# Kernel tuning notes

Measured on AMD Instinct MI355X. Metric: run time of the kernel, lower is better.

## Reference

```python
import jax, jax.numpy as jnp
import numpy as np

B, S, T, D = 4, 512, 512, 256


def setup_inputs() -> dict:
    key = jax.random.key(0)
    ks = jax.random.split(key, 10)
    scale = 1.0 / np.sqrt(D)
    return {
        "source": jax.random.normal(ks[0], (B, S, D), jnp.float32),
        "target": jax.random.normal(ks[1], (B, T, D), jnp.float32),
        "W_src": jax.random.uniform(ks[2], (D, D), jnp.float32, -scale, scale),
        "b_src": jax.random.uniform(ks[3], (D,), jnp.float32, -scale, scale),
        "W_tgt": jax.random.uniform(ks[4], (D, D), jnp.float32, -scale, scale),
        "b_tgt": jax.random.uniform(ks[5], (D,), jnp.float32, -scale, scale),
        "W_res": jax.random.uniform(ks[6], (D, 1), jnp.float32, -scale, scale),
        "b_res": jax.random.uniform(ks[7], (1,), jnp.float32, -scale, scale),
        "W_prob": jax.random.uniform(ks[8], (D, 2), jnp.float32, -scale, scale),
        "b_prob": jax.random.uniform(ks[9], (2,), jnp.float32, -scale, scale),
    }


def reference(source, target, W_src, b_src, W_tgt, b_tgt, W_res, b_res, W_prob, b_prob):
    # source: (B,S,D), target: (B,T,D)
    src_lin = jnp.einsum("bsd,de->bse", source, W_src) + b_src  # (B,S,D)
    tgt_lin = jnp.einsum("btd,de->bte", target, W_tgt) + b_tgt  # (B,T,D)
    # Bahdanau-style additive attention: (B,T,S,D) broadcast, tanh, D->1
    h = jnp.tanh(src_lin[:, None, :, :] + tgt_lin[:, :, None, :])  # (B,T,S,D)
    genP = jnp.einsum("btsd,d->bts", h, W_res[:, 0]) + b_res[0]     # (B,T,S)
    prob = jax.nn.softmax(jnp.einsum("btd,de->bte", target, W_prob) + b_prob, axis=-1)  # (B,T,2)
    return genP, prob
```

## Files before the change

kernel.cpp:

```cpp
#include <hip/hip_runtime.h>

#define B_ 4
#define S_ 512
#define T_ 512
#define D_ 256
#define NSRC (B_ * S_)
#define K2F 2.8853900817779268f

typedef __attribute__((ext_vector_type(8))) short short8;
typedef __attribute__((ext_vector_type(4))) float f32x4;
typedef __attribute__((ext_vector_type(2))) float f32x2;

__device__ __forceinline__ unsigned short f2bf(float f) {
    union { float f; unsigned u; } v; v.f = f;
    unsigned r = v.u + 0x7FFF + ((v.u >> 16) & 1);
    return (unsigned short)(r >> 16);
}

__global__ __launch_bounds__(256) void prep_kernel(
    const float* __restrict__ src, const float* __restrict__ tgt,
    const float* __restrict__ Wsrc, const float* __restrict__ Wtgt,
    const float* __restrict__ Wp, const float* __restrict__ bp,
    unsigned short* __restrict__ abf, unsigned short* __restrict__ wtb,
    float* __restrict__ out)
{
    __shared__ float tl[64 * 65];
    const int blk = blockIdx.x, tid = threadIdx.x;

    if (blk < 1024) {
        int i4 = blk * 256 + tid;
        const int half = NSRC * D_ / 4;
        const float4* in = (i4 < half) ? (const float4*)src : (const float4*)tgt;
        int j = (i4 < half) ? i4 : i4 - half;
        float4 v = in[j];
        ushort4 o;
        o.x = f2bf(v.x); o.y = f2bf(v.y); o.z = f2bf(v.z); o.w = f2bf(v.w);
        *(ushort4*)&abf[i4 * 4] = o;
    } else if (blk < 1056) {
        int wb = blk - 1024;
        int e = wb >> 4, ti = wb & 15, tr = ti >> 2, tc = ti & 3;
        int r0 = tr * 64, c0 = tc * 64;
        const float* W = e ? Wtgt : Wsrc;
        #pragma unroll
        for (int it = 0; it < 4; it++) {
            int rr = (tid >> 4) + it * 16;
            int cc = (tid & 15) * 4;
            float4 v = *(const float4*)&W[(r0 + rr) * D_ + c0 + cc];
            tl[(cc + 0) * 65 + rr] = v.x;
            tl[(cc + 1) * 65 + rr] = v.y;
            tl[(cc + 2) * 65 + rr] = v.z;
            tl[(cc + 3) * 65 + rr] = v.w;
        }
        __syncthreads();
        #pragma unroll
        for (int it = 0; it < 2; it++) {
            int jj = (tid >> 3) + it * 32;
            int kk = (tid & 7) * 8;
            ushort4 lo, hi;
            lo.x = f2bf(tl[jj * 65 + kk + 0]); lo.y = f2bf(tl[jj * 65 + kk + 1]);
            lo.z = f2bf(tl[jj * 65 + kk + 2]); lo.w = f2bf(tl[jj * 65 + kk + 3]);
            hi.x = f2bf(tl[jj * 65 + kk + 4]); hi.y = f2bf(tl[jj * 65 + kk + 5]);
            hi.z = f2bf(tl[jj * 65 + kk + 6]); hi.w = f2bf(tl[jj * 65 + kk + 7]);
            int idx = (e * 256 + c0 + jj) * D_ + r0 + kk;
            *(ushort4*)&wtb[idx] = lo;
            *(ushort4*)&wtb[idx + 4] = hi;
        }
    } else {
        int row  = (blk - 1056) * 4 + (tid >> 6);
        int lane = tid & 63;
        float p0 = 0.f, p1 = 0.f;
        #pragma unroll
        for (int i = 0; i < 4; i++) {
            int d = lane + i * 64;
            float v = tgt[row * D_ + d];
            float2 w = *(const float2*)&Wp[d * 2];
            p0 = fmaf(v, w.x, p0);
            p1 = fmaf(v, w.y, p1);
        }
        #pragma unroll
        for (int off = 32; off > 0; off >>= 1) {
            p0 += __shfl_down(p0, off, 64);
            p1 += __shfl_down(p1, off, 64);
        }
        if (lane == 0) {
            const float L2E = 1.4426950408889634f;
            float l0 = p0 + bp[0], l1 = p1 + bp[1];
            float e10 = __builtin_amdgcn_exp2f((l1 - l0) * L2E);
            float e01 = __builtin_amdgcn_exp2f((l0 - l1) * L2E);
            out[B_ * T_ * S_ + row * 2 + 0] = __builtin_amdgcn_rcpf(1.f + e10);
            out[B_ * T_ * S_ + row * 2 + 1] = __builtin_amdgcn_rcpf(1.f + e01);
        }
    }
}

__global__ __launch_bounds__(256) void linT_kernel(
    const unsigned short* __restrict__ abf, const unsigned short* __restrict__ wtb,
    const float* __restrict__ bsrc, const float* __restrict__ btgt,
    float* __restrict__ yaT, float* __restrict__ ycT)
{
    int wid  = blockIdx.x * 4 + (threadIdx.x >> 6);
    int lane = threadIdx.x & 63;
    int rg = wid >> 3;
    int cg = wid & 7;
    int e  = rg >> 7;
    int r0 = rg * 16;
    int n = lane & 15, quad = lane >> 4;

    const float* bias = e ? btgt : bsrc;
    float* outT = e ? ycT : yaT;
    int orow0 = r0 - e * NSRC;

    int ct0 = cg * 2, ct1 = cg * 2 + 1;
    f32x4 acc0 = {0.f, 0.f, 0.f, 0.f};
    f32x4 acc1 = {0.f, 0.f, 0.f, 0.f};

    const unsigned short* aP  = &abf[(r0 + n) * D_ + quad * 8];
    const unsigned short* b0P = &wtb[(e * 256 + ct0 * 16 + n) * D_ + quad * 8];
    const unsigned short* b1P = &wtb[(e * 256 + ct1 * 16 + n) * D_ + quad * 8];

    #pragma unroll
    for (int ks = 0; ks < 8; ks++) {
        short8 a  = *(const short8*)&aP[ks * 32];
        short8 b0 = *(const short8*)&b0P[ks * 32];
        short8 b1 = *(const short8*)&b1P[ks * 32];
        acc0 = __builtin_amdgcn_mfma_f32_16x16x32_bf16(a, b0, acc0, 0, 0, 0);
        acc1 = __builtin_amdgcn_mfma_f32_16x16x32_bf16(a, b1, acc1, 0, 0, 0);
    }

    float b0v = bias[ct0 * 16 + n];
    float b1v = bias[ct1 * 16 + n];
    float4 o0, o1;
    o0.x = __builtin_amdgcn_exp2f((acc0[0] + b0v) * K2F);
    o0.y = __builtin_amdgcn_exp2f((acc0[1] + b0v) * K2F);
    o0.z = __builtin_amdgcn_exp2f((acc0[2] + b0v) * K2F);
    o0.w = __builtin_amdgcn_exp2f((acc0[3] + b0v) * K2F);
    o1.x = __builtin_amdgcn_exp2f((acc1[0] + b1v) * K2F);
    o1.y = __builtin_amdgcn_exp2f((acc1[1] + b1v) * K2F);
    o1.z = __builtin_amdgcn_exp2f((acc1[2] + b1v) * K2F);
    o1.w = __builtin_amdgcn_exp2f((acc1[3] + b1v) * K2F);
    *(float4*)&outT[(ct0 * 16 + n) * NSRC + orow0 + quad * 4] = o0;
    *(float4*)&outT[(ct1 * 16 + n) * NSRC + orow0 + quad * 4] = o1;
}

#define GSTR 68
__global__ __launch_bounds__(1024, 4) void genp_kernel(
    const float* __restrict__ yaT, const float* __restrict__ ycT,
    const float* __restrict__ Wres, const float* __restrict__ bres,
    float* __restrict__ out)
{
    __shared__ float lbuf[2 * 64 * GSTR];
    float* ls = lbuf;
    float* lt = lbuf + 64 * GSTR;
    __shared__ float c0s;

    const int tid = threadIdx.x;
    const int lane = tid & 63, w = tid >> 6;
    const int s0 = blockIdx.x * 64;
    const int t0 = blockIdx.y * 64;
    const int b  = blockIdx.z;
    const int sg = b * S_ + s0;
    const int tg = b * T_ + t0;

    if (w == 0) {
        float s = Wres[lane] + Wres[lane + 64] + Wres[lane + 128] + Wres[lane + 192];
        #pragma unroll
        for (int off = 32; off > 0; off >>= 1) s += __shfl_xor(s, off, 64);
        if (lane == 0) c0s = s + bres[0];
    }

    const int q = w >> 2;
    const int m = lane & 15;
    const int g = (w & 3) * 4 + (lane >> 4);
    const int dbase = q * 16;

    f32x2 acc[4][2];
    #pragma unroll
    for (int i = 0; i < 4; i++) {
        acc[i][0] = (f32x2){0.f, 0.f};
        acc[i][1] = (f32x2){0.f, 0.f};
    }

    for (int c = 0; c < 4; c++) {
        __syncthreads();
        #pragma unroll
        for (int j = 0; j < 8; j++) {
            int r = w * 8 + j;
            if (r < 64) ls[r * GSTR + lane] = yaT[(c * 64 + r) * NSRC + sg + lane];
            else        lt[(r - 64) * GSTR + lane] = ycT[(c * 64 + r - 64) * NSRC + tg + lane];
        }
        __syncthreads();

        const float* wp = &Wres[c * 64 + dbase];
        const f32x2 one2 = {1.f, 1.f};
        #pragma unroll
        for (int kp = 0; kp < 8; kp++) {
            const int d0 = dbase + 2 * kp, d1 = d0 + 1;
            float4 av0 = *(const float4*)&ls[d0 * GSTR + 4 * m];
            float4 av1 = *(const float4*)&ls[d1 * GSTR + 4 * m];
            float4 cv0 = *(const float4*)&lt[d0 * GSTR + 4 * g];
            float4 cv1 = *(const float4*)&lt[d1 * GSTR + 4 * g];
            const float w0 = wp[2 * kp], w1 = wp[2 * kp + 1];
            const f32x2 w0v = {w0, w0}, w1v = {w1, w1};
            f32x2 a0p[2] = {{av0.x, av0.y}, {av0.z, av0.w}};
            f32x2 a1p[2] = {{av1.x, av1.y}, {av1.z, av1.w}};
            const float cc0[4] = {cv0.x, cv0.y, cv0.z, cv0.w};
            const float cc1[4] = {cv1.x, cv1.y, cv1.z, cv1.w};
            #pragma unroll
            for (int i = 0; i < 4; i++) {
                const f32x2 c0v = {cc0[i], cc0[i]};
                const f32x2 c1v = {cc1[i], cc1[i]};
                #pragma unroll
                for (int jp = 0; jp < 2; jp++) {
                    f32x2 dd0 = a0p[jp] * c0v + one2;
                    f32x2 dd1 = a1p[jp] * c1v + one2;
                    f32x2 den = dd0 * dd1;
                    f32x2 tnu = dd0 * w1v;
                    f32x2 num = dd1 * w0v + tnu;
                    f32x2 r;
                    r.x = __builtin_amdgcn_rcpf(den.x);
                    r.y = __builtin_amdgcn_rcpf(den.y);
                    acc[i][jp] = num * r + acc[i][jp];
                }
            }
        }
    }

    __syncthreads();
    const int slot = ((w & 3) * 64 + lane) * 17;
    const int slotH = ((q >> 1) * 256 + (w & 3) * 64 + lane) * 17;
    if (q == 1 || q == 3) {
        #pragma unroll
        for (int i = 0; i < 4; i++) {
            float4 p = {acc[i][0].x, acc[i][0].y, acc[i][1].x, acc[i][1].y};
            *(float4*)&lbuf[slotH + 4 * i] = p;
        }
    }
    __syncthreads();
    if (q == 0 || q == 2) {
        #pragma unroll
        for (int i = 0; i < 4; i++) {
            float4 p = *(const float4*)&lbuf[slotH + 4 * i];
            acc[i][0].x += p.x; acc[i][0].y += p.y;
            acc[i][1].x += p.z; acc[i][1].y += p.w;
        }
    }
    __syncthreads();
    if (q == 2) {
        #pragma unroll
        for (int i = 0; i < 4; i++) {
            float4 p = {acc[i][0].x, acc[i][0].y, acc[i][1].x, acc[i][1].y};
            *(float4*)&lbuf[slot + 4 * i] = p;
        }
    }
    __syncthreads();
    if (q == 0) {
        const float C0 = c0s;
        #pragma unroll
        for (int i = 0; i < 4; i++) {
            float4 p = *(const float4*)&lbuf[slot + 4 * i];
            float4 o;
            o.x = C0 - 2.f * (acc[i][0].x + p.x);
            o.y = C0 - 2.f * (acc[i][0].y + p.y);
            o.z = C0 - 2.f * (acc[i][1].x + p.z);
            o.w = C0 - 2.f * (acc[i][1].y + p.w);
            *(float4*)&out[(b * T_ + t0 + 4 * g + i) * S_ + s0 + 4 * m] = o;
        }
    }
}

extern "C" void kernel_launch(void* const* d_in, const int* in_sizes, int n_in,
                              void* d_out, int out_size, void* d_ws, size_t ws_size,
                              hipStream_t stream) {
    const float* source = (const float*)d_in[0];
    const float* target = (const float*)d_in[1];
    const float* W_src  = (const float*)d_in[2];
    const float* b_src  = (const float*)d_in[3];
    const float* W_tgt  = (const float*)d_in[4];
    const float* b_tgt  = (const float*)d_in[5];
    const float* W_res  = (const float*)d_in[6];
    const float* b_res  = (const float*)d_in[7];
    const float* W_prob = (const float*)d_in[8];
    const float* b_prob = (const float*)d_in[9];
    float* out = (float*)d_out;

    unsigned short* abf = (unsigned short*)d_ws;
    unsigned short* wtb = abf + 2 * NSRC * D_;
    float* yaT = (float*)(wtb + 2 * D_ * D_);
    float* ycT = yaT + D_ * NSRC;

    prep_kernel<<<1568, 256, 0, stream>>>(source, target, W_src, W_tgt,
                                          W_prob, b_prob, abf, wtb, out);
    linT_kernel<<<512, 256, 0, stream>>>(abf, wtb, b_src, b_tgt, yaT, ycT);
    genp_kernel<<<dim3(8, 8, 4), 1024, 0, stream>>>(yaT, ycT, W_res, b_res, out);
}
```

Measured before the change: 118.8 us.

## Restructure linear MFMA tiles to keep weight fragments in registers across row tiles

The linear-projection kernel now swaps MFMA operands so the weight tile sits in the A slot. Each wave loads a 16-column weight slice once into registers and reuses it across four 16-row activation tiles, instead of loading one activation tile and two weight tiles per wave. The transposed outputs are now written as coalesced scalar stores along the row dimension, and the grid is halved. This reduces redundant weight loads and improves store coalescing, at the cost of fewer waves in flight for latency hiding.

```diff
diff --git a/kernel.cpp b/kernel.cpp
--- a/kernel.cpp
+++ b/kernel.cpp
@@ -98,48 +98,41 @@
     const float* __restrict__ bsrc, const float* __restrict__ btgt,
     float* __restrict__ yaT, float* __restrict__ ycT)
 {
-    int wid  = blockIdx.x * 4 + (threadIdx.x >> 6);
-    int lane = threadIdx.x & 63;
-    int rg = wid >> 3;
-    int cg = wid & 7;
-    int e  = rg >> 7;
-    int r0 = rg * 16;
-    int n = lane & 15, quad = lane >> 4;
+    const int W    = blockIdx.x * 4 + (threadIdx.x >> 6);
+    const int lane = threadIdx.x & 63;
+    const int rgrp = W >> 4;
+    const int dg   = W & 15;
+    const int e    = rgrp >> 5;
+    const int R0   = rgrp * 64;
+    const int orow0 = R0 - e * NSRC;
+    const int d0   = dg * 16;
+    const int n = lane & 15, quad = lane >> 4;
 
     const float* bias = e ? btgt : bsrc;
     float* outT = e ? ycT : yaT;
-    int orow0 = r0 - e * NSRC;
-
-    int ct0 = cg * 2, ct1 = cg * 2 + 1;
-    f32x4 acc0 = {0.f, 0.f, 0.f, 0.f};
-    f32x4 acc1 = {0.f, 0.f, 0.f, 0.f};
-
-    const unsigned short* aP  = &abf[(r0 + n) * D_ + quad * 8];
-    const unsigned short* b0P = &wtb[(e * 256 + ct0 * 16 + n) * D_ + quad * 8];
-    const unsigned short* b1P = &wtb[(e * 256 + ct1 * 16 + n) * D_ + quad * 8];
-
+
+    const unsigned short* aP = &wtb[(e * 256 + d0 + n) * D_ + quad * 8];
+    short8 af[8];
     #pragma unroll
-    for (int ks = 0; ks < 8; ks++) {
-        short8 a  = *(const short8*)&aP[ks * 32];
-        short8 b0 = *(const short8*)&b0P[ks * 32];
-        short8 b1 = *(const short8*)&b1P[ks * 32];
-        acc0 = __builtin_amdgcn_mfma_f32_16x16x32_bf16(a, b0, acc0, 0, 0, 0);
-        acc1 = __builtin_amdgcn_mfma_f32_16x16x32_bf16(a, b1, acc1, 0, 0, 0);
-    }
-
-    float b0v = bias[ct0 * 16 + n];
-    float b1v = bias[ct1 * 16 + n];
-    float4 o0, o1;
-    o0.x = __builtin_amdgcn_exp2f((acc0[0] + b0v) * K2F);
-    o0.y = __builtin_amdgcn_exp2f((acc0[1] + b0v) * K2F);
-    o0.z = __builtin_amdgcn_exp2f((acc0[2] + b0v) * K2F);
-    o0.w = __builtin_amdgcn_exp2f((acc0[3] + b0v) * K2F);
-    o1.x = __builtin_amdgcn_exp2f((acc1[0] + b1v) * K2F);
-    o1.y = __builtin_amdgcn_exp2f((acc1[1] + b1v) * K2F);
-    o1.z = __builtin_amdgcn_exp2f((acc1[2] + b1v) * K2F);
-    o1.w = __builtin_amdgcn_exp2f((acc1[3] + b1v) * K2F);
-    *(float4*)&outT[(ct0 * 16 + n) * NSRC + orow0 + quad * 4] = o0;
-    *(float4*)&outT[(ct1 * 16 + n) * NSRC + orow0 + quad * 4] = o1;
+    for (int ks = 0; ks < 8; ks++) af[ks] = *(const short8*)&aP[ks * 32];
+
+    const float4 vb = *(const float4*)&bias[d0 + quad * 4];
+
+    #pragma unroll
+    for (int f = 0; f < 4; f++) {
+        const unsigned short* bP = &abf[(R0 + 16 * f + n) * D_ + quad * 8];
+        f32x4 acc = {0.f, 0.f, 0.f, 0.f};
+        #pragma unroll
+        for (int ks = 0; ks < 8; ks++) {
+            short8 bf = *(const short8*)&bP[ks * 32];
+            acc = __builtin_amdgcn_mfma_f32_16x16x32_bf16(af[ks], bf, acc, 0, 0, 0);
+        }
+        const int rbase = orow0 + 16 * f + n;
+        outT[(d0 + quad * 4 + 0) * NSRC + rbase] = __builtin_amdgcn_exp2f((acc[0] + vb.x) * K2F);
+        outT[(d0 + quad * 4 + 1) * NSRC + rbase] = __builtin_amdgcn_exp2f((acc[1] + vb.y) * K2F);
+        outT[(d0 + quad * 4 + 2) * NSRC + rbase] = __builtin_amdgcn_exp2f((acc[2] + vb.z) * K2F);
+        outT[(d0 + quad * 4 + 3) * NSRC + rbase] = __builtin_amdgcn_exp2f((acc[3] + vb.w) * K2F);
+    }
 }
 
 #define GSTR 68
@@ -290,6 +283,6 @@
 
     prep_kernel<<<1568, 256, 0, stream>>>(source, target, W_src, W_tgt,
                                           W_prob, b_prob, abf, wtb, out);
-    linT_kernel<<<512, 256, 0, stream>>>(abf, wtb, b_src, b_tgt, yaT, ycT);
+    linT_kernel<<<256, 256, 0, stream>>>(abf, wtb, b_src, b_tgt, yaT, ycT);
     genp_kernel<<<dim3(8, 8, 4), 1024, 0, stream>>>(yaT, ycT, W_res, b_res, out);
 }
```

New measurement: 116.6 us. No clear change (-1.9%).
